# Kernel optimization log

Hardware: AMD Instinct MI355X
Metric: run time of the kernel (lower is better)

## Reference

```python
import jax, jax.numpy as jnp
import numpy as np

DIM = 512
N_HEADS = 8
HEAD_DIM = DIM // N_HEADS


def setup_inputs() -> dict:
    key = jax.random.key(0)
    ks = jax.random.split(key, 7)
    b, l, m = 4, 2048, 2048
    scale = 1.0 / np.sqrt(DIM)
    return {
        "q": jax.random.normal(ks[0], (b, l, DIM), dtype=jnp.float32),
        "k": jax.random.normal(ks[1], (b, m, DIM), dtype=jnp.float32),
        "v": jax.random.normal(ks[2], (b, m, DIM), dtype=jnp.float32),
        "w_q": jax.random.normal(ks[3], (DIM, DIM), dtype=jnp.float32) * scale,
        "w_k": jax.random.normal(ks[4], (DIM, DIM), dtype=jnp.float32) * scale,
        "w_v": jax.random.normal(ks[5], (DIM, DIM), dtype=jnp.float32) * scale,
        "w_o": jax.random.normal(ks[6], (DIM, DIM), dtype=jnp.float32) * scale,
    }


def reference(q, k, v, w_q, w_k, w_v, w_o):
    b, l, _ = q.shape
    m = k.shape[1]
    # Linear projections (weights stored as [in, out])
    qp = (q @ w_q).reshape(b, l, HEAD_DIM, N_HEADS)
    kp = (k @ w_k).reshape(b, m, HEAD_DIM, N_HEADS)
    vp = (v @ w_v).reshape(b, m, HEAD_DIM, N_HEADS)  # computed but unused, as in source
    # Explicit score matrix [b, l, m, n] — matches source einsum
    score = jnp.einsum('bldn,bmdn->blmn', qp, kp) / np.sqrt(HEAD_DIM)
    attn = jax.nn.softmax(score, axis=2)  # softmax over m (dim=2 in source)
    # NOTE: source contracts attention weights with k (not v) — reproduced faithfully.
    x = jnp.einsum('blmn,bmdn->bldn', attn, kp)
    x = x.reshape(b, l, HEAD_DIM * N_HEADS)  # 'b l d n -> b l (d n)'
    return x @ w_o
```

## Files before the change

kernel.cpp:

```cpp
#include <hip/hip_runtime.h>
#include <hip/hip_bf16.h>

#define DIM 512
#define NH 8
#define HD 64
#define BATCH 4
#define SEQ 2048
#define ROWS (BATCH * SEQ)

typedef float f32x4 __attribute__((ext_vector_type(4)));
typedef __bf16 bf16x8 __attribute__((ext_vector_type(8)));
typedef short s16x8 __attribute__((ext_vector_type(8)));

#define QSCALE (0.125f * 1.4426950408889634f)

__device__ __forceinline__ short f2bf(float f) {
    unsigned u = __builtin_bit_cast(unsigned, f);
    u += 0x7fff + ((u >> 16) & 1);
    return (short)(u >> 16);
}

__device__ __forceinline__ f32x4 mfma16(s16x8 a, s16x8 b, f32x4 c) {
    return __builtin_amdgcn_mfma_f32_16x16x32_bf16(
        __builtin_bit_cast(bf16x8, a), __builtin_bit_cast(bf16x8, b), c, 0, 0, 0);
}

__global__ __launch_bounds__(256) void proj_kernel(
    const float* __restrict__ Xq, const float* __restrict__ Wq, short* __restrict__ Yq,
    const float* __restrict__ Xk, const float* __restrict__ Wk, short* __restrict__ Yk)
{
    __shared__ short Alds[64][72];
    __shared__ short Btlds[64][72];
    __shared__ short Ylds[64][64];

    const float* X = blockIdx.z ? Xk : Xq;
    const float* W = blockIdx.z ? Wk : Wq;
    short*       Y = blockIdx.z ? Yk : Yq;
    const float escale = blockIdx.z ? 1.0f : QSCALE;

    const int bm = blockIdx.x;
    const int bn = blockIdx.y;
    const int tid = threadIdx.x;
    const int w = tid >> 6;
    const int lane = tid & 63;
    const int l15 = lane & 15;
    const int hi = lane >> 4;

    const int row0 = bm * 64;
    const int ar = tid >> 2;
    const int aj = (tid & 3) * 16;
    const int bcg = tid & 63;
    const int bkg = tid >> 6;

    const float* asrc = X + (size_t)(row0 + ar) * DIM + aj;
    const float* bsrc = W + (size_t)(bkg * 16) * DIM + bn * 64 + bcg;

    f32x4 acc[4];
#pragma unroll
    for (int t = 0; t < 4; ++t) acc[t] = (f32x4){0.f, 0.f, 0.f, 0.f};

    f32x4 av[4];
    float bw[16];
#pragma unroll
    for (int j = 0; j < 4; ++j) av[j] = *(const f32x4*)(asrc + j * 4);
#pragma unroll
    for (int i = 0; i < 16; ++i) bw[i] = bsrc[(size_t)i * DIM];

    for (int kc = 0; kc < DIM / 64; ++kc) {
        {
            s16x8 pa0, pa1;
#pragma unroll
            for (int i = 0; i < 4; ++i) {
                pa0[i] = f2bf(av[0][i]); pa0[i + 4] = f2bf(av[1][i]);
                pa1[i] = f2bf(av[2][i]); pa1[i + 4] = f2bf(av[3][i]);
            }
            *(s16x8*)&Alds[ar][aj]     = pa0;
            *(s16x8*)&Alds[ar][aj + 8] = pa1;
        }
        {
            s16x8 pb0, pb1;
#pragma unroll
            for (int i = 0; i < 8; ++i) { pb0[i] = f2bf(bw[i]); pb1[i] = f2bf(bw[8 + i]); }
            *(s16x8*)&Btlds[bcg][bkg * 16]     = pb0;
            *(s16x8*)&Btlds[bcg][bkg * 16 + 8] = pb1;
        }
        __syncthreads();
        if (kc + 1 < DIM / 64) {
#pragma unroll
            for (int j = 0; j < 4; ++j)
                av[j] = *(const f32x4*)(asrc + (kc + 1) * 64 + j * 4);
#pragma unroll
            for (int i = 0; i < 16; ++i)
                bw[i] = bsrc[(size_t)((kc + 1) * 64 + i) * DIM];
        }
        s16x8 a0 = *(const s16x8*)&Alds[w * 16 + l15][hi * 8];
        s16x8 a1 = *(const s16x8*)&Alds[w * 16 + l15][32 + hi * 8];
#pragma unroll
        for (int t = 0; t < 4; ++t) {
            s16x8 b0 = *(const s16x8*)&Btlds[t * 16 + l15][hi * 8];
            s16x8 b1 = *(const s16x8*)&Btlds[t * 16 + l15][32 + hi * 8];
            acc[t] = mfma16(a1, b1, mfma16(a0, b0, acc[t]));
        }
        __syncthreads();
    }

#pragma unroll
    for (int t = 0; t < 4; ++t)
#pragma unroll
        for (int r = 0; r < 4; ++r)
            Ylds[w * 16 + hi * 4 + r][t * 16 + l15] = f2bf(acc[t][r] * escale);
    __syncthreads();

    for (int task = tid; task < 512; task += 256) {
        const int lr = task >> 3;
        const int n  = task & 7;
        const int gr = row0 + lr;
        const int b  = gr >> 11;
        const int l  = gr & 2047;
        s16x8 vv;
#pragma unroll
        for (int i = 0; i < 8; ++i) vv[i] = Ylds[lr][i * 8 + n];
        *(s16x8*)&Y[(((size_t)(b * NH + n)) * SEQ + l) * HD + bn * 8] = vv;
    }
}

__global__ __launch_bounds__(512) void attn_kernel(
    const short* __restrict__ Qh, const short* __restrict__ Kh,
    short* __restrict__ Xh)
{
    __shared__ short Klds[64][72];
    __shared__ short Ktlds[64][72];
    __shared__ short Plds[8][16][72];

    const int qt  = blockIdx.x;
    const int hb  = blockIdx.y;
    const int tid = threadIdx.x;
    const int w = tid >> 6, lane = tid & 63, l15 = lane & 15, hi = lane >> 4;

    const size_t kbase = (size_t)hb * SEQ * HD;
    const size_t qbase = kbase + (size_t)qt * 128 * HD;

    const short* qrow = Qh + qbase + (size_t)(w * 16 + l15) * HD + hi * 8;
    const s16x8 qa0 = *(const s16x8*)(qrow);
    const s16x8 qa1 = *(const s16x8*)(qrow + 32);

    f32x4 o[4];
#pragma unroll
    for (int t = 0; t < 4; ++t) o[t] = (f32x4){0.f, 0.f, 0.f, 0.f};
    float m2[4], lsum[4];
#pragma unroll
    for (int r = 0; r < 4; ++r) { m2[r] = -1e30f; lsum[r] = 0.f; }

    const int sr = tid >> 3;
    const int sj = (tid & 7) * 8;
    const short* ksrc = Kh + kbase + (size_t)sr * HD + sj;
    const int cd = tid & 63;
    const int cm = (tid >> 6) * 8;
    const short* csrc = Kh + kbase + (size_t)cm * HD + cd;

    s16x8 strow = *(const s16x8*)(ksrc);
    s16x8 scol;
#pragma unroll
    for (int i = 0; i < 8; ++i) scol[i] = csrc[(size_t)i * HD];

    for (int mc = 0; mc < SEQ / 64; ++mc) {
        *(s16x8*)&Klds[sr][sj]   = strow;
        *(s16x8*)&Ktlds[cd][cm]  = scol;
        __syncthreads();
        if (mc + 1 < SEQ / 64) {
            const short* rn = ksrc + (size_t)(mc + 1) * 64 * HD;
            strow = *(const s16x8*)(rn);
            const short* cn = csrc + (size_t)(mc + 1) * 64 * HD;
#pragma unroll
            for (int i = 0; i < 8; ++i) scol[i] = cn[(size_t)i * HD];
        }

        f32x4 s[4];
#pragma unroll
        for (int t = 0; t < 4; ++t) {
            s[t] = (f32x4){0.f, 0.f, 0.f, 0.f};
            s16x8 b0 = *(const s16x8*)&Klds[t * 16 + l15][hi * 8];
            s16x8 b1 = *(const s16x8*)&Klds[t * 16 + l15][32 + hi * 8];
            s[t] = mfma16(qa0, b0, s[t]);
            s[t] = mfma16(qa1, b1, s[t]);
        }

#pragma unroll
        for (int r = 0; r < 4; ++r) {
            float v = fmaxf(fmaxf(s[0][r], s[1][r]), fmaxf(s[2][r], s[3][r]));
            v = fmaxf(v, __shfl_xor(v, 1));
            v = fmaxf(v, __shfl_xor(v, 2));
            v = fmaxf(v, __shfl_xor(v, 4));
            v = fmaxf(v, __shfl_xor(v, 8));
            const float mn = fmaxf(m2[r], v);
            const float fc = __builtin_amdgcn_exp2f(m2[r] - mn);
            m2[r] = mn;
            lsum[r] *= fc;
            o[0][r] *= fc; o[1][r] *= fc; o[2][r] *= fc; o[3][r] *= fc;
        }
#pragma unroll
        for (int r = 0; r < 4; ++r) {
            float ps = 0.f;
#pragma unroll
            for (int t = 0; t < 4; ++t) {
                float p = __builtin_amdgcn_exp2f(s[t][r] - m2[r]);
                ps += p;
                Plds[w][hi * 4 + r][t * 16 + l15] = f2bf(p);
            }
            ps += __shfl_xor(ps, 1);
            ps += __shfl_xor(ps, 2);
            ps += __shfl_xor(ps, 4);
            ps += __shfl_xor(ps, 8);
            lsum[r] += ps;
        }

#pragma unroll
        for (int ks = 0; ks < 2; ++ks) {
            s16x8 a = *(const s16x8*)&Plds[w][l15][ks * 32 + hi * 8];
#pragma unroll
            for (int t = 0; t < 4; ++t) {
                s16x8 b = *(const s16x8*)&Ktlds[t * 16 + l15][ks * 32 + hi * 8];
                o[t] = mfma16(a, b, o[t]);
            }
        }
        __syncthreads();
    }

#pragma unroll
    for (int r = 0; r < 4; ++r) {
        const float rcp = 1.0f / lsum[r];
        const size_t rowoff = qbase + (size_t)(w * 16 + hi * 4 + r) * HD;
#pragma unroll
        for (int t = 0; t < 4; ++t)
            Xh[rowoff + t * 16 + l15] = f2bf(o[t][r] * rcp);
    }
}

__global__ __launch_bounds__(256) void out_kernel(
    const short* __restrict__ Xh, const float* __restrict__ W,
    float* __restrict__ Out)
{
    __shared__ short Alds[64][72];
    __shared__ short Btlds[64][72];

    const int bm = blockIdx.x;
    const int bn = blockIdx.y;
    const int tid = threadIdx.x;
    const int w = tid >> 6, lane = tid & 63, l15 = lane & 15, hi = lane >> 4;

    const int row0 = bm * 64;
    const int bcg = tid & 63;
    const int bkg = tid >> 6;
    const float* bsrc = W + (size_t)(bkg * 16) * DIM + bn * 64 + bcg;

    const int lr0 = tid >> 3,          n0 = tid & 7;
    const int lr1 = (tid + 256) >> 3,  n1 = tid & 7;
    const int gr0 = row0 + lr0, gr1 = row0 + lr1;
    const short* ag0 = Xh + (((size_t)((gr0 >> 11) * NH + n0)) * SEQ + (gr0 & 2047)) * HD;
    const short* ag1 = Xh + (((size_t)((gr1 >> 11) * NH + n1)) * SEQ + (gr1 & 2047)) * HD;

    f32x4 acc[4];
#pragma unroll
    for (int t = 0; t < 4; ++t) acc[t] = (f32x4){0.f, 0.f, 0.f, 0.f};

    float bw[16];
#pragma unroll
    for (int i = 0; i < 16; ++i) bw[i] = bsrc[(size_t)i * DIM];
    s16x8 av0 = *(const s16x8*)(ag0);
    s16x8 av1 = *(const s16x8*)(ag1);

    for (int kc = 0; kc < DIM / 64; ++kc) {
        {
#pragma unroll
            for (int i = 0; i < 8; ++i) Alds[lr0][i * 8 + n0] = av0[i];
#pragma unroll
            for (int i = 0; i < 8; ++i) Alds[lr1][i * 8 + n1] = av1[i];
        }
        {
            s16x8 pb0, pb1;
#pragma unroll
            for (int i = 0; i < 8; ++i) { pb0[i] = f2bf(bw[i]); pb1[i] = f2bf(bw[8 + i]); }
            *(s16x8*)&Btlds[bcg][bkg * 16]     = pb0;
            *(s16x8*)&Btlds[bcg][bkg * 16 + 8] = pb1;
        }
        __syncthreads();
        if (kc + 1 < DIM / 64) {
#pragma unroll
            for (int i = 0; i < 16; ++i)
                bw[i] = bsrc[(size_t)((kc + 1) * 64 + i) * DIM];
            av0 = *(const s16x8*)(ag0 + (kc + 1) * 8);
            av1 = *(const s16x8*)(ag1 + (kc + 1) * 8);
        }
        s16x8 a0 = *(const s16x8*)&Alds[w * 16 + l15][hi * 8];
        s16x8 a1 = *(const s16x8*)&Alds[w * 16 + l15][32 + hi * 8];
#pragma unroll
        for (int t = 0; t < 4; ++t) {
            s16x8 b0 = *(const s16x8*)&Btlds[t * 16 + l15][hi * 8];
            s16x8 b1 = *(const s16x8*)&Btlds[t * 16 + l15][32 + hi * 8];
            acc[t] = mfma16(a1, b1, mfma16(a0, b0, acc[t]));
        }
        __syncthreads();
    }

#pragma unroll
    for (int t = 0; t < 4; ++t)
#pragma unroll
        for (int r = 0; r < 4; ++r)
            Out[(size_t)(row0 + w * 16 + hi * 4 + r) * DIM + bn * 64 + t * 16 + l15] =
                acc[t][r];
}

extern "C" void kernel_launch(void* const* d_in, const int* in_sizes, int n_in,
                              void* d_out, int out_size, void* d_ws, size_t ws_size,
                              hipStream_t stream) {
    const float* q   = (const float*)d_in[0];
    const float* k   = (const float*)d_in[1];
    const float* w_q = (const float*)d_in[3];
    const float* w_k = (const float*)d_in[4];
    const float* w_o = (const float*)d_in[6];
    float* out = (float*)d_out;

    short* qh = (short*)d_ws;
    short* kh = qh + (size_t)ROWS * DIM;
    short* xh = kh + (size_t)ROWS * DIM;

    proj_kernel<<<dim3(ROWS / 64, DIM / 64, 2), 256, 0, stream>>>(
        q, w_q, qh, k, w_k, kh);
    attn_kernel<<<dim3(SEQ / 128, BATCH * NH), 512, 0, stream>>>(qh, kh, xh);
    out_kernel<<<dim3(ROWS / 64, DIM / 64), 256, 0, stream>>>(xh, w_o, out);
}
```

Before: 252.0 us.

## Split attention over key range with merge kernel and MFMA row sums

Adds a split-KV (flash-decoding style) path: the key sequence is split into two halves across a third grid dimension, each block writes unnormalized fp32 partial outputs plus running max and sum, and a new merge kernel combines them into bf16 output. This doubles the number of attention blocks (512 to 1024) to fill more compute units on the GPU. It also replaces the shuffle-based softmax row-sum reduction with an MFMA against a vector of ones. In exchange it adds extra global traffic for the partials and an extra kernel launch, and it only runs if the workspace is large enough.

```diff
diff --git a/kernel.cpp b/kernel.cpp
--- a/kernel.cpp
+++ b/kernel.cpp
@@ -11,6 +11,7 @@
 typedef float f32x4 __attribute__((ext_vector_type(4)));
 typedef __bf16 bf16x8 __attribute__((ext_vector_type(8)));
 typedef short s16x8 __attribute__((ext_vector_type(8)));
+typedef short s16x4 __attribute__((ext_vector_type(4)));
 
 #define QSCALE (0.125f * 1.4426950408889634f)
 
@@ -124,9 +125,11 @@
     }
 }
 
+template <bool SPLIT>
 __global__ __launch_bounds__(512) void attn_kernel(
     const short* __restrict__ Qh, const short* __restrict__ Kh,
-    short* __restrict__ Xh)
+    short* __restrict__ Xh, float* __restrict__ PO, float* __restrict__ PM,
+    int cps)
 {
     __shared__ short Klds[64][72];
     __shared__ short Ktlds[64][72];
@@ -134,6 +137,7 @@
 
     const int qt  = blockIdx.x;
     const int hb  = blockIdx.y;
+    const int sl  = blockIdx.z;
     const int tid = threadIdx.x;
     const int w = tid >> 6, lane = tid & 63, l15 = lane & 15, hi = lane >> 4;
 
@@ -144,30 +148,36 @@
     const s16x8 qa0 = *(const s16x8*)(qrow);
     const s16x8 qa1 = *(const s16x8*)(qrow + 32);
 
+    s16x8 ones;
+#pragma unroll
+    for (int i = 0; i < 8; ++i) ones[i] = (short)0x3F80;
+
     f32x4 o[4];
 #pragma unroll
     for (int t = 0; t < 4; ++t) o[t] = (f32x4){0.f, 0.f, 0.f, 0.f};
-    float m2[4], lsum[4];
-#pragma unroll
-    for (int r = 0; r < 4; ++r) { m2[r] = -1e30f; lsum[r] = 0.f; }
-
+    f32x4 ls = (f32x4){0.f, 0.f, 0.f, 0.f};
+    float m2[4];
+#pragma unroll
+    for (int r = 0; r < 4; ++r) m2[r] = -1e30f;
+
+    const int mc0 = sl * cps;
     const int sr = tid >> 3;
     const int sj = (tid & 7) * 8;
-    const short* ksrc = Kh + kbase + (size_t)sr * HD + sj;
+    const short* ksrc = Kh + kbase + (size_t)(mc0 * 64 + sr) * HD + sj;
     const int cd = tid & 63;
     const int cm = (tid >> 6) * 8;
-    const short* csrc = Kh + kbase + (size_t)cm * HD + cd;
+    const short* csrc = Kh + kbase + (size_t)(mc0 * 64 + cm) * HD + cd;
 
     s16x8 strow = *(const s16x8*)(ksrc);
     s16x8 scol;
 #pragma unroll
     for (int i = 0; i < 8; ++i) scol[i] = csrc[(size_t)i * HD];
 
-    for (int mc = 0; mc < SEQ / 64; ++mc) {
-        *(s16x8*)&Klds[sr][sj]   = strow;
-        *(s16x8*)&Ktlds[cd][cm]  = scol;
-        __syncthreads();
-        if (mc + 1 < SEQ / 64) {
+    for (int mc = 0; mc < cps; ++mc) {
+        *(s16x8*)&Klds[sr][sj]  = strow;
+        *(s16x8*)&Ktlds[cd][cm] = scol;
+        __syncthreads();
+        if (mc + 1 < cps) {
             const short* rn = ksrc + (size_t)(mc + 1) * 64 * HD;
             strow = *(const s16x8*)(rn);
             const short* cn = csrc + (size_t)(mc + 1) * 64 * HD;
@@ -195,28 +205,20 @@
             const float mn = fmaxf(m2[r], v);
             const float fc = __builtin_amdgcn_exp2f(m2[r] - mn);
             m2[r] = mn;
-            lsum[r] *= fc;
+            ls[r] *= fc;
             o[0][r] *= fc; o[1][r] *= fc; o[2][r] *= fc; o[3][r] *= fc;
         }
 #pragma unroll
-        for (int r = 0; r < 4; ++r) {
-            float ps = 0.f;
-#pragma unroll
-            for (int t = 0; t < 4; ++t) {
-                float p = __builtin_amdgcn_exp2f(s[t][r] - m2[r]);
-                ps += p;
-                Plds[w][hi * 4 + r][t * 16 + l15] = f2bf(p);
-            }
-            ps += __shfl_xor(ps, 1);
-            ps += __shfl_xor(ps, 2);
-            ps += __shfl_xor(ps, 4);
-            ps += __shfl_xor(ps, 8);
-            lsum[r] += ps;
-        }
+        for (int r = 0; r < 4; ++r)
+#pragma unroll
+            for (int t = 0; t < 4; ++t)
+                Plds[w][hi * 4 + r][t * 16 + l15] =
+                    f2bf(__builtin_amdgcn_exp2f(s[t][r] - m2[r]));
 
 #pragma unroll
         for (int ks = 0; ks < 2; ++ks) {
             s16x8 a = *(const s16x8*)&Plds[w][l15][ks * 32 + hi * 8];
+            ls = mfma16(a, ones, ls);
 #pragma unroll
             for (int t = 0; t < 4; ++t) {
                 s16x8 b = *(const s16x8*)&Ktlds[t * 16 + l15][ks * 32 + hi * 8];
@@ -226,14 +228,68 @@
         __syncthreads();
     }
 
-#pragma unroll
-    for (int r = 0; r < 4; ++r) {
-        const float rcp = 1.0f / lsum[r];
-        const size_t rowoff = qbase + (size_t)(w * 16 + hi * 4 + r) * HD;
-#pragma unroll
-        for (int t = 0; t < 4; ++t)
-            Xh[rowoff + t * 16 + l15] = f2bf(o[t][r] * rcp);
-    }
+    if (SPLIT) {
+        const size_t poff = ((size_t)sl * (BATCH * NH) + hb) * SEQ * HD +
+                            (size_t)qt * 128 * HD;
+#pragma unroll
+        for (int r = 0; r < 4; ++r) {
+            const int row = w * 16 + hi * 4 + r;
+#pragma unroll
+            for (int t = 0; t < 4; ++t)
+                PO[poff + (size_t)row * HD + t * 16 + l15] = o[t][r];
+        }
+        if (l15 == 0) {
+#pragma unroll
+            for (int r = 0; r < 4; ++r) {
+                const size_t sidx = ((size_t)sl * (BATCH * NH) + hb) * SEQ +
+                                    qt * 128 + w * 16 + hi * 4 + r;
+                PM[sidx * 2]     = m2[r];
+                PM[sidx * 2 + 1] = ls[r];
+            }
+        }
+    } else {
+#pragma unroll
+        for (int r = 0; r < 4; ++r) {
+            const float rcp = 1.0f / ls[r];
+            const size_t rowoff = qbase + (size_t)(w * 16 + hi * 4 + r) * HD;
+#pragma unroll
+            for (int t = 0; t < 4; ++t)
+                Xh[rowoff + t * 16 + l15] = f2bf(o[t][r] * rcp);
+        }
+    }
+}
+
+__global__ __launch_bounds__(256) void merge_kernel(
+    const float* __restrict__ PO, const float* __restrict__ PM,
+    short* __restrict__ Xh, int ns)
+{
+    const int idx = blockIdx.x * 256 + threadIdx.x;
+    const int d4 = idx & 15;
+    const int q  = (idx >> 4) & (SEQ - 1);
+    const int hb = idx >> 15;
+    const size_t row = (size_t)hb * SEQ + q;
+    const size_t SLICE_O = (size_t)(BATCH * NH) * SEQ * HD;
+    const size_t SLICE_S = (size_t)(BATCH * NH) * SEQ;
+
+    float M = -1e30f;
+    for (int i = 0; i < ns; ++i)
+        M = fmaxf(M, PM[(i * SLICE_S + row) * 2]);
+    float L = 0.f;
+    f32x4 O = (f32x4){0.f, 0.f, 0.f, 0.f};
+    for (int i = 0; i < ns; ++i) {
+        const float mi = PM[(i * SLICE_S + row) * 2];
+        const float li = PM[(i * SLICE_S + row) * 2 + 1];
+        const float wgt = __builtin_amdgcn_exp2f(mi - M);
+        L += li * wgt;
+        f32x4 po = *(const f32x4*)&PO[i * SLICE_O + row * HD + d4 * 4];
+#pragma unroll
+        for (int j = 0; j < 4; ++j) O[j] += po[j] * wgt;
+    }
+    const float rl = 1.0f / L;
+    s16x4 pk;
+#pragma unroll
+    for (int j = 0; j < 4; ++j) pk[j] = f2bf(O[j] * rl);
+    *(s16x4*)&Xh[row * HD + d4 * 4] = pk;
 }
 
 __global__ __launch_bounds__(256) void out_kernel(
@@ -323,9 +379,24 @@
     short* qh = (short*)d_ws;
     short* kh = qh + (size_t)ROWS * DIM;
     short* xh = kh + (size_t)ROWS * DIM;
+    const size_t base_bytes = (size_t)3 * ROWS * DIM * sizeof(short);
+    float* po = (float*)((char*)d_ws + base_bytes);
+    float* pm = po + (size_t)2 * (BATCH * NH) * SEQ * HD;
+    const size_t need2 = base_bytes +
+        (size_t)2 * (BATCH * NH) * SEQ * HD * 4 +
+        (size_t)2 * (BATCH * NH) * SEQ * 2 * 4;
+    const int ns = (ws_size >= need2) ? 2 : 1;
 
     proj_kernel<<<dim3(ROWS / 64, DIM / 64, 2), 256, 0, stream>>>(
         q, w_q, qh, k, w_k, kh);
-    attn_kernel<<<dim3(SEQ / 128, BATCH * NH), 512, 0, stream>>>(qh, kh, xh);
+    if (ns == 2) {
+        attn_kernel<true><<<dim3(SEQ / 128, BATCH * NH, 2), 512, 0, stream>>>(
+            qh, kh, xh, po, pm, (SEQ / 64) / 2);
+        merge_kernel<<<(BATCH * NH) * SEQ * (HD / 4) / 256, 256, 0, stream>>>(
+            po, pm, xh, 2);
+    } else {
+        attn_kernel<false><<<dim3(SEQ / 128, BATCH * NH, 1), 512, 0, stream>>>(
+            qh, kh, xh, nullptr, nullptr, SEQ / 64);
+    }
     out_kernel<<<dim3(ROWS / 64, DIM / 64), 256, 0, stream>>>(xh, w_o, out);
 }
```

New measurement: 246.2 us. -2.3%, faster.
